# Performance work log

Measured on AMD Instinct MI355X. Metric: run time of the kernel, lower is better.

## Reference

```python
import jax, jax.numpy as jnp
import numpy as np

IN_F, OUT_F = 256, 256
GRID, ORDER = 5, 3
K = GRID + ORDER + 1  # 9 knots
EPS_MINMAX = 1e-7     # K.epsilon()
EPS_BN = 1e-3         # keras BatchNormalization default epsilon


def setup_inputs() -> dict:
    key = jax.random.key(0)
    ks = jax.random.split(key, 4)
    x = jax.random.normal(ks[0], (32, 32, 32, IN_F), dtype=jnp.float32)
    he = lambda k, shape, fan_in: jax.random.normal(k, shape, jnp.float32) * np.sqrt(2.0 / fan_in)
    base_weight = he(ks[1], (IN_F, OUT_F), IN_F)
    spline_weight = he(ks[2], (OUT_F, IN_F, K), IN_F * K)
    spline_scaler = jnp.ones((OUT_F, IN_F), jnp.float32)
    return {
        'x': x,
        'base_weight': base_weight,
        'spline_weight': spline_weight,
        'spline_scaler': spline_scaler,
        'bn_base_gamma': jnp.ones((OUT_F,), jnp.float32),
        'bn_base_beta': jnp.zeros((OUT_F,), jnp.float32),
        'bn_base_mean': jnp.zeros((OUT_F,), jnp.float32),
        'bn_base_var': jnp.ones((OUT_F,), jnp.float32),
        'bn_spline_gamma': jnp.ones((OUT_F,), jnp.float32),
        'bn_spline_beta': jnp.zeros((OUT_F,), jnp.float32),
        'bn_spline_mean': jnp.zeros((OUT_F,), jnp.float32),
        'bn_spline_var': jnp.ones((OUT_F,), jnp.float32),
    }


def _bn(z, gamma, beta, mean, var):
    # Keras BatchNormalization, inference mode (training=False)
    return gamma * (z - mean) * jax.lax.rsqrt(var + EPS_BN) + beta


def reference(x, base_weight, spline_weight, spline_scaler,
              bn_base_gamma, bn_base_beta, bn_base_mean, bn_base_var,
              bn_spline_gamma, bn_spline_beta, bn_spline_mean, bn_spline_var):
    B, H, W, _ = x.shape
    xf = x.reshape(-1, IN_F)  # [N, in]

    # base path: GEMM -> BN -> SiLU
    base = xf @ base_weight
    base = jax.nn.silu(_bn(base, bn_base_gamma, bn_base_beta, bn_base_mean, bn_base_var))

    # min-max normalize per feature over the flattened batch
    x_min = jnp.min(xf, axis=0, keepdims=True)
    x_max = jnp.max(xf, axis=0, keepdims=True)
    xn = (xf - x_min) / (x_max - x_min + EPS_MINMAX)

    # triangle basis: relu(1 - |x - knot|), knots = linspace(-1, 1, K)
    knots = jnp.linspace(-1.0, 1.0, K, dtype=jnp.float32)
    basis = jnp.maximum(0.0, 1.0 - jnp.abs(xn[:, :, None] - knots[None, None, :]))  # [N, in, K]

    # scaled spline weight, flattened GEMM
    w = (spline_weight * spline_scaler[:, :, None]).reshape(OUT_F, IN_F * K)  # [out, in*K]
    spline = basis.reshape(-1, IN_F * K) @ w.T  # [N, out]
    spline = _bn(spline, bn_spline_gamma, bn_spline_beta, bn_spline_mean, bn_spline_var)

    out = base + spline
    return out.reshape(B, H, W, OUT_F)
```

## Files before the change

### kernel.cpp

```cpp
#include <hip/hip_runtime.h>
#include <stdint.h>
#include <stddef.h>

typedef _Float16 h2 __attribute__((ext_vector_type(2)));
typedef _Float16 h8 __attribute__((ext_vector_type(8)));
typedef float f4 __attribute__((ext_vector_type(4)));

union Hfrag { h2 p[4]; h8 v; };

#define WS_PMIN   0
#define WS_PMAX   524288
#define WS_BT     0
#define WS_SMALL  1048576
#define WS_SCALEV (WS_SMALL + 0)
#define WS_BKN    (WS_SMALL + 1024)
#define WS_C0     (WS_SMALL + 3072)
#define WS_BSC    (WS_SMALL + 4096)
#define WS_BSH    (WS_SMALL + 5120)
#define WS_SSC    (WS_SMALL + 6144)
#define WS_SSH    (WS_SMALL + 7168)

__global__ __launch_bounds__(256) void kan_minmax(const float* __restrict__ x,
                                                  float* __restrict__ pmin,
                                                  float* __restrict__ pmax) {
  __shared__ f4 smn[4][64], smx[4][64];
  const int b = blockIdx.x, t = threadIdx.x;
  const int fq = t & 63, rg = t >> 6;
  const float* p = x + (size_t)b * 64 * 256 + (size_t)rg * 16 * 256 + fq * 4;
  f4 mn = (f4)(3.402823466e38f), mx = (f4)(-3.402823466e38f);
#pragma unroll
  for (int j = 0; j < 16; ++j) {
    f4 v = *(const f4*)(p + (size_t)j * 256);
    mn = __builtin_elementwise_min(mn, v);
    mx = __builtin_elementwise_max(mx, v);
  }
  smn[rg][fq] = mn; smx[rg][fq] = mx;
  __syncthreads();
  if (rg == 0) {
#pragma unroll
    for (int g = 1; g < 4; ++g) {
      mn = __builtin_elementwise_min(mn, smn[g][fq]);
      mx = __builtin_elementwise_max(mx, smx[g][fq]);
    }
    *(f4*)(pmin + (size_t)b * 256 + fq * 4) = mn;
    *(f4*)(pmax + (size_t)b * 256 + fq * 4) = mx;
  }
}

__global__ __launch_bounds__(256) void kan_finalize(
    const float* __restrict__ pmin, const float* __restrict__ pmax,
    const float* __restrict__ g1, const float* __restrict__ b1,
    const float* __restrict__ m1, const float* __restrict__ v1,
    const float* __restrict__ g2, const float* __restrict__ b2,
    const float* __restrict__ m2, const float* __restrict__ v2,
    float* __restrict__ scalev, _Float16* __restrict__ bkn,
    float* __restrict__ bscv, float* __restrict__ bshv,
    float* __restrict__ sscv, float* __restrict__ sshv) {
  __shared__ f4 smn[256], smx[256];
  const int t = threadIdx.x, q = blockIdx.x;
  const float* pm = pmin + (size_t)t * 256 + q * 4;
  const float* px = pmax + (size_t)t * 256 + q * 4;
  f4 mn = __builtin_elementwise_min(*(const f4*)pm, *(const f4*)(pm + 256 * 256));
  f4 mx = __builtin_elementwise_max(*(const f4*)px, *(const f4*)(px + 256 * 256));
  smn[t] = mn; smx[t] = mx;
  __syncthreads();
  for (int st = 128; st > 0; st >>= 1) {
    if (t < st) {
      smn[t] = __builtin_elementwise_min(smn[t], smn[t + st]);
      smx[t] = __builtin_elementwise_max(smx[t], smx[t + st]);
    }
    __syncthreads();
  }
  if (t == 0) {
    const f4 fmn = smn[0], fmx = smx[0];
#pragma unroll
    for (int j = 0; j < 4; ++j) {
      const int o = q * 4 + j;
      const float mnS = fmn[j], mxS = fmx[j];
      const float rng = mxS - mnS + 1e-7f;
      scalev[o] = 1.0f / rng;
      const float step = 0.25f * rng;
#pragma unroll
      for (int jj = 0; jj < 4; ++jj)
        bkn[jj * 256 + o] = (_Float16)(mnS + step * (float)jj);
      const float bs = g1[o] / sqrtf(v1[o] + 1e-3f);
      bscv[o] = bs;
      bshv[o] = b1[o] - m1[o] * bs;
      const float ss = g2[o] / sqrtf(v2[o] + 1e-3f);
      sscv[o] = ss;
      sshv[o] = b2[o] - m2[o] * ss;
    }
  }
}

__global__ __launch_bounds__(256) void kan_buildw(
    const float* __restrict__ spline_w, const float* __restrict__ spline_s,
    const float* __restrict__ base_w, const float* __restrict__ scalev,
    _Float16* __restrict__ Bt, float* __restrict__ C0) {
  const int og = blockIdx.x;
  const int i  = threadIdx.x;
  const float* wp = spline_w + (size_t)(og * 256 + i) * 9;
  const float w1 = wp[1], w2 = wp[2], w3 = wp[3], w4 = wp[4];
  const float w5 = wp[5], w6 = wp[6], w7 = wp[7], w8 = wp[8];
  const float s  = spline_s[og * 256 + i];
  const float sc = scalev[i];
  const float wp0 = 0.25f*w1 + 0.5f*w2 + 0.75f*w3 + w4 + 0.75f*w5 + 0.5f*w6 + 0.25f*w7;
  float wj[4];
  wj[0] = (w5 + w6 + w7 + w8) - (w1 + w2 + w3 + w4);
  wj[1] = w1 - 2.0f * w5;
  wj[2] = w2 - 2.0f * w6;
  wj[3] = w3 - 2.0f * w7;
  const float ssc = s * sc;
  const int half = og >> 7, o = og & 127, ic = i >> 5, kk = i & 31;
#pragma unroll
  for (int j = 0; j < 4; ++j) {
    const int ks = j * 8 + ic;
    Bt[((size_t)(ks * 2 + half) * 128 + o) * 32 + kk] = (_Float16)(wj[j] * ssc);
  }
  Bt[((size_t)((32 + ic) * 2 + half) * 128 + o) * 32 + kk] =
      (_Float16)base_w[(size_t)i * 256 + og];
  __shared__ float red[256];
  red[i] = wp0 * s;
  __syncthreads();
  for (int st = 128; st > 0; st >>= 1) {
    if (i < st) red[i] += red[i + st];
    __syncthreads();
  }
  if (i == 0) C0[og] = red[0];
}

__global__ __launch_bounds__(256, 2) void kan_gemm(
    const float* __restrict__ x, const _Float16* __restrict__ Bt,
    const _Float16* __restrict__ bkn, const float* __restrict__ C0,
    const float* __restrict__ bscv, const float* __restrict__ bshv,
    const float* __restrict__ sscv, const float* __restrict__ sshv,
    float* __restrict__ out) {
  const int tid = threadIdx.x;
  const int lane = tid & 63;
  const int wv = tid >> 6;
  const int wm = wv >> 1, wn = wv & 1;
  const int lr = lane & 15, lg = lane >> 4;
  const int mt = blockIdx.x & 255, nt = blockIdx.x >> 8;

  const int rowA = mt * 128 + wm * 64 + lr;
  const int colB = wn * 64 + lr;

  f4 accS[4][4], accB[4][4];
#pragma unroll
  for (int m = 0; m < 4; ++m)
#pragma unroll
    for (int n = 0; n < 4; ++n) { accS[m][n] = (f4)0.0f; accB[m][n] = (f4)0.0f; }

  const char* btbase = (const char*)Bt + (size_t)nt * 8192 + (size_t)colB * 64 + (size_t)lg * 16;

  h2 hz; hz[0] = (_Float16)0.0f; hz[1] = (_Float16)0.0f;

  f4 xa[4], xb[4];
  {
    const int ib = lg * 8;
#pragma unroll
    for (int m = 0; m < 4; ++m) {
      const float* px = x + (size_t)(rowA + m * 16) * 256 + ib;
      xa[m] = *(const f4*)px; xb[m] = *(const f4*)(px + 4);
    }
  }

#define SPLINE_STEP(J, BF)                                                   \
  {                                                                          \
    Hfrag bbj;                                                               \
    bbj.v = *(const h8*)(bkn + (J) * 256 + ic * 32 + lg * 8);                \
    _Pragma("unroll")                                                        \
    for (int m = 0; m < 4; ++m) {                                            \
      Hfrag afm;                                                             \
      _Pragma("unroll")                                                      \
      for (int qq = 0; qq < 4; ++qq) {                                       \
        h2 d = xh[m].p[qq] - bbj.p[qq];                                      \
        afm.p[qq] = __builtin_elementwise_max(d, hz);                        \
      }                                                                      \
      _Pragma("unroll")                                                      \
      for (int n = 0; n < 4; ++n)                                            \
        accS[m][n] = __builtin_amdgcn_mfma_f32_16x16x32_f16(afm.v, BF[n].v,  \
                                                            accS[m][n], 0, 0, 0); \
    }                                                                        \
  }

#define LOADB(BF, BYTEOFF)                                                   \
  _Pragma("unroll")                                                          \
  for (int n = 0; n < 4; ++n)                                                \
    BF[n].v = *(const h8*)(bpic + (BYTEOFF) + n * 1024);

#pragma unroll 1
  for (int ic = 0; ic < 8; ++ic) {
    const char* bpic = btbase + (size_t)ic * 16384;

    Hfrag bfA[4], bfB[4];
    LOADB(bfA, 0)

    Hfrag xh[4];
#pragma unroll
    for (int m = 0; m < 4; ++m) {
      xh[m].p[0][0] = (_Float16)xa[m].x; xh[m].p[0][1] = (_Float16)xa[m].y;
      xh[m].p[1][0] = (_Float16)xa[m].z; xh[m].p[1][1] = (_Float16)xa[m].w;
      xh[m].p[2][0] = (_Float16)xb[m].x; xh[m].p[2][1] = (_Float16)xb[m].y;
      xh[m].p[3][0] = (_Float16)xb[m].z; xh[m].p[3][1] = (_Float16)xb[m].w;
    }

    LOADB(bfB, 131072)
    SPLINE_STEP(0, bfA)
    LOADB(bfA, 262144)
    SPLINE_STEP(1, bfB)
    LOADB(bfB, 393216)
    SPLINE_STEP(2, bfA)
    LOADB(bfA, 524288)
    SPLINE_STEP(3, bfB)

#pragma unroll
    for (int m = 0; m < 4; ++m)
#pragma unroll
      for (int n = 0; n < 4; ++n)
        accB[m][n] = __builtin_amdgcn_mfma_f32_16x16x32_f16(xh[m].v, bfA[n].v, accB[m][n], 0, 0, 0);

    __builtin_amdgcn_sched_barrier(0);
    if (ic < 7) {
      const int ib = (ic + 1) * 32 + lg * 8;
#pragma unroll
      for (int m = 0; m < 4; ++m) {
        const float* px = x + (size_t)(rowA + m * 16) * 256 + ib;
        xa[m] = *(const f4*)px; xb[m] = *(const f4*)(px + 4);
      }
    }
  }
#undef SPLINE_STEP
#undef LOADB

#pragma unroll
  for (int n = 0; n < 4; ++n) {
    const int col = nt * 128 + colB + n * 16;
    const float vbs = bscv[col], vbh = bshv[col];
    const float vss = sscv[col];
    const float vsh = sshv[col] + vss * C0[col];
#pragma unroll
    for (int m = 0; m < 4; ++m) {
      const int row0 = mt * 128 + wm * 64 + m * 16 + lg * 4;
#pragma unroll
      for (int r = 0; r < 4; ++r) {
        const float zb = accB[m][n][r] * vbs + vbh;
        const float si = zb / (1.0f + __expf(-zb));
        const float val = si + accS[m][n][r] * vss + vsh;
        out[(size_t)(row0 + r) * 256 + col] = val;
      }
    }
  }
}

extern "C" void kernel_launch(void* const* d_in, const int* in_sizes, int n_in,
                              void* d_out, int out_size, void* d_ws, size_t ws_size,
                              hipStream_t stream) {
  const float* x        = (const float*)d_in[0];
  const float* base_w   = (const float*)d_in[1];
  const float* spline_w = (const float*)d_in[2];
  const float* spline_s = (const float*)d_in[3];
  const float* g1 = (const float*)d_in[4];
  const float* b1 = (const float*)d_in[5];
  const float* m1 = (const float*)d_in[6];
  const float* v1 = (const float*)d_in[7];
  const float* g2 = (const float*)d_in[8];
  const float* b2 = (const float*)d_in[9];
  const float* m2 = (const float*)d_in[10];
  const float* v2 = (const float*)d_in[11];
  float* out = (float*)d_out;
  char* ws = (char*)d_ws;

  float* pmin     = (float*)(ws + WS_PMIN);
  float* pmax     = (float*)(ws + WS_PMAX);
  _Float16* Bt    = (_Float16*)(ws + WS_BT);
  float* scalev   = (float*)(ws + WS_SCALEV);
  _Float16* bkn   = (_Float16*)(ws + WS_BKN);
  float* C0       = (float*)(ws + WS_C0);
  float* bscv     = (float*)(ws + WS_BSC);
  float* bshv     = (float*)(ws + WS_BSH);
  float* sscv     = (float*)(ws + WS_SSC);
  float* sshv     = (float*)(ws + WS_SSH);

  kan_minmax<<<512, 256, 0, stream>>>(x, pmin, pmax);
  kan_finalize<<<64, 256, 0, stream>>>(pmin, pmax, g1, b1, m1, v1, g2, b2, m2, v2,
                                       scalev, bkn, bscv, bshv, sscv, sshv);
  kan_buildw<<<256, 256, 0, stream>>>(spline_w, spline_s, base_w, scalev, Bt, C0);
  kan_gemm<<<512, 256, 0, stream>>>(x, Bt, bkn, C0, bscv, bshv, sscv, sshv, out);
}
```

Before: 151.2 us.

## Use atomic min/max reduction, fold finalize into buildw, halve GEMM M tile

Replaces the two-stage min/max reduction with order-preserving integer atomics into a global buffer initialised by memsets. This removes the finalize kernel, and its per-feature setup moves into the weight-building kernel. The GEMM tile shrinks from 128 to 64 rows, so there are twice as many blocks and the occupancy hint rises to 3. Knot offsets are staged in shared memory, and the next x prefetch is moved ahead of the last spline step to hide load latency. The costs are atomic contention, two extra memset launches, and more redundant B-fragment loads per output row.

```diff
diff --git a/kernel.cpp b/kernel.cpp
--- a/kernel.cpp
+++ b/kernel.cpp
@@ -8,21 +8,29 @@
 
 union Hfrag { h2 p[4]; h8 v; };
 
-#define WS_PMIN   0
-#define WS_PMAX   524288
 #define WS_BT     0
-#define WS_SMALL  1048576
-#define WS_SCALEV (WS_SMALL + 0)
-#define WS_BKN    (WS_SMALL + 1024)
-#define WS_C0     (WS_SMALL + 3072)
-#define WS_BSC    (WS_SMALL + 4096)
-#define WS_BSH    (WS_SMALL + 5120)
-#define WS_SSC    (WS_SMALL + 6144)
-#define WS_SSH    (WS_SMALL + 7168)
+#define WS_SMALL  655360
+#define WS_GMIN   (WS_SMALL + 0)
+#define WS_GMAX   (WS_SMALL + 1024)
+#define WS_BKN    (WS_SMALL + 2048)
+#define WS_C0     (WS_SMALL + 4096)
+#define WS_BSC    (WS_SMALL + 5120)
+#define WS_BSH    (WS_SMALL + 6144)
+#define WS_SSC    (WS_SMALL + 7168)
+#define WS_SSH    (WS_SMALL + 8192)
+
+__device__ __forceinline__ unsigned int fenc(float f) {
+  int b = __float_as_int(f);
+  return (unsigned int)(b >= 0 ? (b | 0x80000000) : ~b);
+}
+__device__ __forceinline__ float fdec(unsigned int u) {
+  int b = (u & 0x80000000u) ? (int)(u & 0x7FFFFFFFu) : ~(int)u;
+  return __int_as_float(b);
+}
 
 __global__ __launch_bounds__(256) void kan_minmax(const float* __restrict__ x,
-                                                  float* __restrict__ pmin,
-                                                  float* __restrict__ pmax) {
+                                                  unsigned int* __restrict__ gmin,
+                                                  unsigned int* __restrict__ gmax) {
   __shared__ f4 smn[4][64], smx[4][64];
   const int b = blockIdx.x, t = threadIdx.x;
   const int fq = t & 63, rg = t >> 6;
@@ -42,68 +50,49 @@
       mn = __builtin_elementwise_min(mn, smn[g][fq]);
       mx = __builtin_elementwise_max(mx, smx[g][fq]);
     }
-    *(f4*)(pmin + (size_t)b * 256 + fq * 4) = mn;
-    *(f4*)(pmax + (size_t)b * 256 + fq * 4) = mx;
-  }
-}
-
-__global__ __launch_bounds__(256) void kan_finalize(
-    const float* __restrict__ pmin, const float* __restrict__ pmax,
+#pragma unroll
+    for (int j = 0; j < 4; ++j) {
+      atomicMin(gmin + fq * 4 + j, fenc(mn[j]));
+      atomicMax(gmax + fq * 4 + j, fenc(mx[j]));
+    }
+  }
+}
+
+__global__ __launch_bounds__(256) void kan_buildw(
+    const float* __restrict__ spline_w, const float* __restrict__ spline_s,
+    const float* __restrict__ base_w,
+    const unsigned int* __restrict__ gmin, const unsigned int* __restrict__ gmax,
     const float* __restrict__ g1, const float* __restrict__ b1,
     const float* __restrict__ m1, const float* __restrict__ v1,
     const float* __restrict__ g2, const float* __restrict__ b2,
     const float* __restrict__ m2, const float* __restrict__ v2,
-    float* __restrict__ scalev, _Float16* __restrict__ bkn,
+    _Float16* __restrict__ Bt, _Float16* __restrict__ bkn, float* __restrict__ C0,
     float* __restrict__ bscv, float* __restrict__ bshv,
     float* __restrict__ sscv, float* __restrict__ sshv) {
-  __shared__ f4 smn[256], smx[256];
-  const int t = threadIdx.x, q = blockIdx.x;
-  const float* pm = pmin + (size_t)t * 256 + q * 4;
-  const float* px = pmax + (size_t)t * 256 + q * 4;
-  f4 mn = __builtin_elementwise_min(*(const f4*)pm, *(const f4*)(pm + 256 * 256));
-  f4 mx = __builtin_elementwise_max(*(const f4*)px, *(const f4*)(px + 256 * 256));
-  smn[t] = mn; smx[t] = mx;
-  __syncthreads();
-  for (int st = 128; st > 0; st >>= 1) {
-    if (t < st) {
-      smn[t] = __builtin_elementwise_min(smn[t], smn[t + st]);
-      smx[t] = __builtin_elementwise_max(smx[t], smx[t + st]);
-    }
-    __syncthreads();
-  }
-  if (t == 0) {
-    const f4 fmn = smn[0], fmx = smx[0];
-#pragma unroll
-    for (int j = 0; j < 4; ++j) {
-      const int o = q * 4 + j;
-      const float mnS = fmn[j], mxS = fmx[j];
-      const float rng = mxS - mnS + 1e-7f;
-      scalev[o] = 1.0f / rng;
-      const float step = 0.25f * rng;
-#pragma unroll
-      for (int jj = 0; jj < 4; ++jj)
-        bkn[jj * 256 + o] = (_Float16)(mnS + step * (float)jj);
-      const float bs = g1[o] / sqrtf(v1[o] + 1e-3f);
-      bscv[o] = bs;
-      bshv[o] = b1[o] - m1[o] * bs;
-      const float ss = g2[o] / sqrtf(v2[o] + 1e-3f);
-      sscv[o] = ss;
-      sshv[o] = b2[o] - m2[o] * ss;
-    }
-  }
-}
-
-__global__ __launch_bounds__(256) void kan_buildw(
-    const float* __restrict__ spline_w, const float* __restrict__ spline_s,
-    const float* __restrict__ base_w, const float* __restrict__ scalev,
-    _Float16* __restrict__ Bt, float* __restrict__ C0) {
   const int og = blockIdx.x;
   const int i  = threadIdx.x;
+  const float mnI = fdec(gmin[i]);
+  const float mxI = fdec(gmax[i]);
+  const float rng = mxI - mnI + 1e-7f;
+  const float sc = 1.0f / rng;
+  if (og == 0) {
+    const float step = 0.25f * rng;
+#pragma unroll
+    for (int j = 0; j < 4; ++j)
+      bkn[j * 256 + i] = (_Float16)(mnI + step * (float)j);
+  }
+  if (i == 0) {
+    const float bs = g1[og] / sqrtf(v1[og] + 1e-3f);
+    bscv[og] = bs;
+    bshv[og] = b1[og] - m1[og] * bs;
+    const float ss = g2[og] / sqrtf(v2[og] + 1e-3f);
+    sscv[og] = ss;
+    sshv[og] = b2[og] - m2[og] * ss;
+  }
   const float* wp = spline_w + (size_t)(og * 256 + i) * 9;
   const float w1 = wp[1], w2 = wp[2], w3 = wp[3], w4 = wp[4];
   const float w5 = wp[5], w6 = wp[6], w7 = wp[7], w8 = wp[8];
   const float s  = spline_s[og * 256 + i];
-  const float sc = scalev[i];
   const float wp0 = 0.25f*w1 + 0.5f*w2 + 0.75f*w3 + w4 + 0.75f*w5 + 0.5f*w6 + 0.25f*w7;
   float wj[4];
   wj[0] = (w5 + w6 + w7 + w8) - (w1 + w2 + w3 + w4);
@@ -129,7 +118,7 @@
   if (i == 0) C0[og] = red[0];
 }
 
-__global__ __launch_bounds__(256, 2) void kan_gemm(
+__global__ __launch_bounds__(256, 3) void kan_gemm(
     const float* __restrict__ x, const _Float16* __restrict__ Bt,
     const _Float16* __restrict__ bkn, const float* __restrict__ C0,
     const float* __restrict__ bscv, const float* __restrict__ bshv,
@@ -140,14 +129,18 @@
   const int wv = tid >> 6;
   const int wm = wv >> 1, wn = wv & 1;
   const int lr = lane & 15, lg = lane >> 4;
-  const int mt = blockIdx.x & 255, nt = blockIdx.x >> 8;
-
-  const int rowA = mt * 128 + wm * 64 + lr;
+  const int mt = blockIdx.x & 511, nt = blockIdx.x >> 9;
+
+  const int rowA = mt * 64 + wm * 32 + lr;
   const int colB = wn * 64 + lr;
 
-  f4 accS[4][4], accB[4][4];
-#pragma unroll
-  for (int m = 0; m < 4; ++m)
+  __shared__ _Float16 sbkn[1024];
+  *(uint2*)(sbkn + tid * 4) = ((const uint2*)bkn)[tid];
+  __syncthreads();
+
+  f4 accS[2][4], accB[2][4];
+#pragma unroll
+  for (int m = 0; m < 2; ++m)
 #pragma unroll
     for (int n = 0; n < 4; ++n) { accS[m][n] = (f4)0.0f; accB[m][n] = (f4)0.0f; }
 
@@ -155,26 +148,29 @@
 
   h2 hz; hz[0] = (_Float16)0.0f; hz[1] = (_Float16)0.0f;
 
-  f4 xa[4], xb[4];
+  f4 xa[2], xb[2];
   {
     const int ib = lg * 8;
 #pragma unroll
-    for (int m = 0; m < 4; ++m) {
+    for (int m = 0; m < 2; ++m) {
       const float* px = x + (size_t)(rowA + m * 16) * 256 + ib;
       xa[m] = *(const f4*)px; xb[m] = *(const f4*)(px + 4);
     }
   }
 
-#define SPLINE_STEP(J, BF)                                                   \
+#define LOADB(BF, BYTEOFF)                                                   \
+  _Pragma("unroll")                                                          \
+  for (int n = 0; n < 4; ++n)                                                \
+    BF[n].v = *(const h8*)(bpic + (BYTEOFF) + n * 1024);
+
+#define SPLINE_STEP(BB, BF)                                                  \
   {                                                                          \
-    Hfrag bbj;                                                               \
-    bbj.v = *(const h8*)(bkn + (J) * 256 + ic * 32 + lg * 8);                \
     _Pragma("unroll")                                                        \
-    for (int m = 0; m < 4; ++m) {                                            \
+    for (int m = 0; m < 2; ++m) {                                            \
       Hfrag afm;                                                             \
       _Pragma("unroll")                                                      \
       for (int qq = 0; qq < 4; ++qq) {                                       \
-        h2 d = xh[m].p[qq] - bbj.p[qq];                                      \
+        h2 d = xh[m].p[qq] - BB.p[qq];                                       \
         afm.p[qq] = __builtin_elementwise_max(d, hz);                        \
       }                                                                      \
       _Pragma("unroll")                                                      \
@@ -184,21 +180,22 @@
     }                                                                        \
   }
 
-#define LOADB(BF, BYTEOFF)                                                   \
-  _Pragma("unroll")                                                          \
-  for (int n = 0; n < 4; ++n)                                                \
-    BF[n].v = *(const h8*)(bpic + (BYTEOFF) + n * 1024);
-
 #pragma unroll 1
   for (int ic = 0; ic < 8; ++ic) {
     const char* bpic = btbase + (size_t)ic * 16384;
 
+    Hfrag bb0, bb1, bb2, bb3;
+    bb0.v = *(const h8*)(sbkn +       ic * 32 + lg * 8);
+    bb1.v = *(const h8*)(sbkn + 256 + ic * 32 + lg * 8);
+    bb2.v = *(const h8*)(sbkn + 512 + ic * 32 + lg * 8);
+    bb3.v = *(const h8*)(sbkn + 768 + ic * 32 + lg * 8);
+
     Hfrag bfA[4], bfB[4];
     LOADB(bfA, 0)
 
-    Hfrag xh[4];
-#pragma unroll
-    for (int m = 0; m < 4; ++m) {
+    Hfrag xh[2];
+#pragma unroll
+    for (int m = 0; m < 2; ++m) {
       xh[m].p[0][0] = (_Float16)xa[m].x; xh[m].p[0][1] = (_Float16)xa[m].y;
       xh[m].p[1][0] = (_Float16)xa[m].z; xh[m].p[1][1] = (_Float16)xa[m].w;
       xh[m].p[2][0] = (_Float16)xb[m].x; xh[m].p[2][1] = (_Float16)xb[m].y;
@@ -206,29 +203,30 @@
     }
 
     LOADB(bfB, 131072)
-    SPLINE_STEP(0, bfA)
+    SPLINE_STEP(bb0, bfA)
     LOADB(bfA, 262144)
-    SPLINE_STEP(1, bfB)
+    SPLINE_STEP(bb1, bfB)
     LOADB(bfB, 393216)
-    SPLINE_STEP(2, bfA)
+    SPLINE_STEP(bb2, bfA)
     LOADB(bfA, 524288)
-    SPLINE_STEP(3, bfB)
-
-#pragma unroll
-    for (int m = 0; m < 4; ++m)
-#pragma unroll
-      for (int n = 0; n < 4; ++n)
-        accB[m][n] = __builtin_amdgcn_mfma_f32_16x16x32_f16(xh[m].v, bfA[n].v, accB[m][n], 0, 0, 0);
 
     __builtin_amdgcn_sched_barrier(0);
     if (ic < 7) {
       const int ib = (ic + 1) * 32 + lg * 8;
 #pragma unroll
-      for (int m = 0; m < 4; ++m) {
+      for (int m = 0; m < 2; ++m) {
         const float* px = x + (size_t)(rowA + m * 16) * 256 + ib;
         xa[m] = *(const f4*)px; xb[m] = *(const f4*)(px + 4);
       }
     }
+
+    SPLINE_STEP(bb3, bfB)
+
+#pragma unroll
+    for (int m = 0; m < 2; ++m)
+#pragma unroll
+      for (int n = 0; n < 4; ++n)
+        accB[m][n] = __builtin_amdgcn_mfma_f32_16x16x32_f16(xh[m].v, bfA[n].v, accB[m][n], 0, 0, 0);
   }
 #undef SPLINE_STEP
 #undef LOADB
@@ -240,8 +238,8 @@
     const float vss = sscv[col];
     const float vsh = sshv[col] + vss * C0[col];
 #pragma unroll
-    for (int m = 0; m < 4; ++m) {
-      const int row0 = mt * 128 + wm * 64 + m * 16 + lg * 4;
+    for (int m = 0; m < 2; ++m) {
+      const int row0 = mt * 64 + wm * 32 + m * 16 + lg * 4;
 #pragma unroll
       for (int r = 0; r < 4; ++r) {
         const float zb = accB[m][n][r] * vbs + vbh;
@@ -271,20 +269,21 @@
   float* out = (float*)d_out;
   char* ws = (char*)d_ws;
 
-  float* pmin     = (float*)(ws + WS_PMIN);
-  float* pmax     = (float*)(ws + WS_PMAX);
-  _Float16* Bt    = (_Float16*)(ws + WS_BT);
-  float* scalev   = (float*)(ws + WS_SCALEV);
-  _Float16* bkn   = (_Float16*)(ws + WS_BKN);
-  float* C0       = (float*)(ws + WS_C0);
-  float* bscv     = (float*)(ws + WS_BSC);
-  float* bshv     = (float*)(ws + WS_BSH);
-  float* sscv     = (float*)(ws + WS_SSC);
-  float* sshv     = (float*)(ws + WS_SSH);
-
-  kan_minmax<<<512, 256, 0, stream>>>(x, pmin, pmax);
-  kan_finalize<<<64, 256, 0, stream>>>(pmin, pmax, g1, b1, m1, v1, g2, b2, m2, v2,
-                                       scalev, bkn, bscv, bshv, sscv, sshv);
-  kan_buildw<<<256, 256, 0, stream>>>(spline_w, spline_s, base_w, scalev, Bt, C0);
-  kan_gemm<<<512, 256, 0, stream>>>(x, Bt, bkn, C0, bscv, bshv, sscv, sshv, out);
-}
+  _Float16* Bt      = (_Float16*)(ws + WS_BT);
+  unsigned int* gmn = (unsigned int*)(ws + WS_GMIN);
+  unsigned int* gmx = (unsigned int*)(ws + WS_GMAX);
+  _Float16* bkn     = (_Float16*)(ws + WS_BKN);
+  float* C0         = (float*)(ws + WS_C0);
+  float* bscv       = (float*)(ws + WS_BSC);
+  float* bshv       = (float*)(ws + WS_BSH);
+  float* sscv       = (float*)(ws + WS_SSC);
+  float* sshv       = (float*)(ws + WS_SSH);
+
+  hipMemsetAsync(ws + WS_GMIN, 0xFF, 1024, stream);
+  hipMemsetAsync(ws + WS_GMAX, 0x00, 1024, stream);
+  kan_minmax<<<512, 256, 0, stream>>>(x, gmn, gmx);
+  kan_buildw<<<256, 256, 0, stream>>>(spline_w, spline_s, base_w, gmn, gmx,
+                                      g1, b1, m1, v1, g2, b2, m2, v2,
+                                      Bt, bkn, C0, bscv, bshv, sscv, sshv);
+  kan_gemm<<<1024, 256, 0, stream>>>(x, Bt, bkn, C0, bscv, bshv, sscv, sshv, out);
+}
```

Result: slower. 204.2 us (+35.1%).
